# Kernel tuning notes

Hardware: AMD Instinct MI355X
Metric: run time of the kernel (lower is better)

## Reference

```python
import jax, jax.numpy as jnp
import numpy as np

# hyperparameters from init_kwargs
S = 1.0        # scale (fixed in module)
L = 0.5        # margin
W_EQ = 1.0
W_INEQ = 1.0

B, C, H, W, N_ANNOS = 32, 2, 480, 640, 4096


def setup_inputs() -> dict:
    key = jax.random.key(0)
    ks = jax.random.split(key, 8)
    prediction = jax.random.normal(ks[0], (B, C, H, W), dtype=jnp.float32)
    # targets columns: [class_a, x_a, y_a, class_b, x_b, y_b, label]
    ca = jax.random.randint(ks[1], (B, N_ANNOS), 0, C)
    xa = jax.random.randint(ks[2], (B, N_ANNOS), 0, W)
    ya = jax.random.randint(ks[3], (B, N_ANNOS), 0, H)
    cb = jax.random.randint(ks[4], (B, N_ANNOS), 0, C)
    xb = jax.random.randint(ks[5], (B, N_ANNOS), 0, W)
    yb = jax.random.randint(ks[6], (B, N_ANNOS), 0, H)
    lab = jax.random.randint(ks[7], (B, N_ANNOS), -1, 2)  # in {-1,0,1}
    targets = jnp.stack([ca, xa, ya, cb, xb, yb, lab], axis=-1).astype(jnp.int64)
    return {"prediction": prediction, "targets": targets}


def reference(prediction, targets):
    # prediction: [B, 2, H, W]; targets: [B, N, 7] int
    b_idx = jnp.arange(prediction.shape[0])[:, None]  # [B,1] broadcast over N
    # gather point-pair predictions: pred[b, class, row(y), col(x)]
    pa = prediction[b_idx, targets[:, :, 0], targets[:, :, 2], targets[:, :, 1]]  # [B,N]
    pb = prediction[b_idx, targets[:, :, 3], targets[:, :, 5], targets[:, :, 4]]  # [B,N]
    diff = pb - pa
    lab_i = targets[:, :, 6]
    lab = lab_i.astype(prediction.dtype)
    ineq_mask = lab_i != 0
    # squared hinge on inequality pairs, squared error on equality pairs
    loss_ineq = jnp.sum(jnp.square(jax.nn.relu(S * L - S * diff * lab)) * ineq_mask)
    loss_eq = jnp.sum(jnp.square(S * diff) * (~ineq_mask))
    num_ineq = jnp.sum(ineq_mask)
    num_eq = jnp.sum(~ineq_mask)
    norm_ineq = jnp.where(num_ineq > 0, 1.0 / jnp.maximum(num_ineq, 1), 0.0)
    norm_eq = jnp.where(num_eq > 0, 1.0 / jnp.maximum(num_eq, 1), 0.0)
    return W_INEQ * norm_ineq * loss_ineq + W_EQ * norm_eq * loss_eq
```

## Files before the change

### kernel.cpp

```cpp
#include <hip/hip_runtime.h>

#define BB 32
#define CC 2
#define HH 480
#define WW 640
#define NA 4096

struct Accum {
    double loss_ineq;
    double loss_eq;
    unsigned long long num_ineq;
};

__global__ __launch_bounds__(256) void lrizz_main(
        const float* __restrict__ pred,
        const int* __restrict__ tgt,
        Accum* __restrict__ acc) {
    const int total = BB * NA;
    int t = blockIdx.x * blockDim.x + threadIdx.x;

    float li = 0.f, le = 0.f;
    int ni = 0;

    if (t < total) {
        int b = t >> 12;
        const int* tp = tgt + (size_t)t * 7;
        int ca = tp[0], xa = tp[1], ya = tp[2];
        int cb = tp[3], xb = tp[4], yb = tp[5];
        int lab = tp[6];

        size_t base = (size_t)b * (CC * HH * WW);
        float pa = pred[base + ((size_t)ca * HH + (size_t)ya) * WW + (size_t)xa];
        float pb = pred[base + ((size_t)cb * HH + (size_t)yb) * WW + (size_t)xb];
        float diff = pb - pa;

        if (lab != 0) {
            float v = 0.5f - diff * (float)lab;
            v = fmaxf(v, 0.f);
            li = v * v;
            ni = 1;
        } else {
            le = diff * diff;
        }
    }

    #pragma unroll
    for (int off = 32; off > 0; off >>= 1) {
        li += __shfl_down(li, off, 64);
        le += __shfl_down(le, off, 64);
        ni += __shfl_down(ni, off, 64);
    }

    __shared__ float s_li[4], s_le[4];
    __shared__ int   s_ni[4];
    int wid  = threadIdx.x >> 6;
    int lane = threadIdx.x & 63;
    if (lane == 0) { s_li[wid] = li; s_le[wid] = le; s_ni[wid] = ni; }
    __syncthreads();

    if (threadIdx.x == 0) {
        float tli = s_li[0] + s_li[1] + s_li[2] + s_li[3];
        float tle = s_le[0] + s_le[1] + s_le[2] + s_le[3];
        int   tni = s_ni[0] + s_ni[1] + s_ni[2] + s_ni[3];
        atomicAdd(&acc->loss_ineq, (double)tli);
        atomicAdd(&acc->loss_eq,  (double)tle);
        atomicAdd(&acc->num_ineq, (unsigned long long)tni);
    }
}

__global__ void lrizz_final(const Accum* __restrict__ acc, float* __restrict__ out) {
    const double total = (double)(BB * NA);
    double ni = (double)acc->num_ineq;
    double ne = total - ni;
    double r = 0.0;
    if (ni > 0.0) r += acc->loss_ineq / ni;
    if (ne > 0.0) r += acc->loss_eq  / ne;
    out[0] = (float)r;
}

extern "C" void kernel_launch(void* const* d_in, const int* in_sizes, int n_in,
                              void* d_out, int out_size, void* d_ws, size_t ws_size,
                              hipStream_t stream) {
    const float* pred = (const float*)d_in[0];
    const int*   tgt  = (const int*)d_in[1];
    float* out = (float*)d_out;
    Accum* acc = (Accum*)d_ws;

    hipMemsetAsync(acc, 0, sizeof(Accum), stream);

    const int total = BB * NA;
    const int block = 256;
    const int grid  = total / block;
    lrizz_main<<<grid, block, 0, stream>>>(pred, tgt, acc);
    lrizz_final<<<1, 1, 0, stream>>>(acc, out);
}
```

Before: 124.3 us.

## Replace global atomics and memset with grid-stride partials and two-stage reduction

The main kernel now uses a fixed grid of 256 blocks with a grid-stride loop. Each block writes a float4 partial sum to workspace instead of issuing three double/u64 atomics per block. A 256-thread final kernel reduces the partials, and the memset launch is removed. The cost this targets is atomic contention and the extra memset launch. In exchange there is less memory-level parallelism per thread, and the count is now accumulated in float, which is exact at this size.

```diff
diff --git a/kernel.cpp b/kernel.cpp
--- a/kernel.cpp
+++ b/kernel.cpp
@@ -6,23 +6,19 @@
 #define WW 640
 #define NA 4096
 
-struct Accum {
-    double loss_ineq;
-    double loss_eq;
-    unsigned long long num_ineq;
-};
+#define GRID1 256
+#define BLOCK1 256
 
-__global__ __launch_bounds__(256) void lrizz_main(
+__global__ __launch_bounds__(BLOCK1) void lrizz_main(
         const float* __restrict__ pred,
         const int* __restrict__ tgt,
-        Accum* __restrict__ acc) {
+        float4* __restrict__ partials) {
     const int total = BB * NA;
-    int t = blockIdx.x * blockDim.x + threadIdx.x;
+    const int stride = GRID1 * BLOCK1;
 
-    float li = 0.f, le = 0.f;
-    int ni = 0;
+    float li = 0.f, le = 0.f, ni = 0.f;
 
-    if (t < total) {
+    for (int t = blockIdx.x * BLOCK1 + threadIdx.x; t < total; t += stride) {
         int b = t >> 12;
         const int* tp = tgt + (size_t)t * 7;
         int ca = tp[0], xa = tp[1], ya = tp[2];
@@ -35,12 +31,11 @@
         float diff = pb - pa;
 
         if (lab != 0) {
-            float v = 0.5f - diff * (float)lab;
-            v = fmaxf(v, 0.f);
-            li = v * v;
-            ni = 1;
+            float v = fmaxf(0.5f - diff * (float)lab, 0.f);
+            li += v * v;
+            ni += 1.f;
         } else {
-            le = diff * diff;
+            le += diff * diff;
         }
     }
 
@@ -51,31 +46,51 @@
         ni += __shfl_down(ni, off, 64);
     }
 
-    __shared__ float s_li[4], s_le[4];
-    __shared__ int   s_ni[4];
+    __shared__ float s_li[4], s_le[4], s_ni[4];
     int wid  = threadIdx.x >> 6;
     int lane = threadIdx.x & 63;
     if (lane == 0) { s_li[wid] = li; s_le[wid] = le; s_ni[wid] = ni; }
     __syncthreads();
 
     if (threadIdx.x == 0) {
-        float tli = s_li[0] + s_li[1] + s_li[2] + s_li[3];
-        float tle = s_le[0] + s_le[1] + s_le[2] + s_le[3];
-        int   tni = s_ni[0] + s_ni[1] + s_ni[2] + s_ni[3];
-        atomicAdd(&acc->loss_ineq, (double)tli);
-        atomicAdd(&acc->loss_eq,  (double)tle);
-        atomicAdd(&acc->num_ineq, (unsigned long long)tni);
+        float4 p;
+        p.x = s_li[0] + s_li[1] + s_li[2] + s_li[3];
+        p.y = s_le[0] + s_le[1] + s_le[2] + s_le[3];
+        p.z = s_ni[0] + s_ni[1] + s_ni[2] + s_ni[3];
+        p.w = 0.f;
+        partials[blockIdx.x] = p;
     }
 }
 
-__global__ void lrizz_final(const Accum* __restrict__ acc, float* __restrict__ out) {
-    const double total = (double)(BB * NA);
-    double ni = (double)acc->num_ineq;
-    double ne = total - ni;
-    double r = 0.0;
-    if (ni > 0.0) r += acc->loss_ineq / ni;
-    if (ne > 0.0) r += acc->loss_eq  / ne;
-    out[0] = (float)r;
+__global__ __launch_bounds__(GRID1) void lrizz_final(
+        const float4* __restrict__ partials,
+        float* __restrict__ out) {
+    float4 p = partials[threadIdx.x];
+    float li = p.x, le = p.y, ni = p.z;
+
+    #pragma unroll
+    for (int off = 32; off > 0; off >>= 1) {
+        li += __shfl_down(li, off, 64);
+        le += __shfl_down(le, off, 64);
+        ni += __shfl_down(ni, off, 64);
+    }
+
+    __shared__ float s_li[4], s_le[4], s_ni[4];
+    int wid  = threadIdx.x >> 6;
+    int lane = threadIdx.x & 63;
+    if (lane == 0) { s_li[wid] = li; s_le[wid] = le; s_ni[wid] = ni; }
+    __syncthreads();
+
+    if (threadIdx.x == 0) {
+        double tli = (double)(s_li[0] + s_li[1] + s_li[2] + s_li[3]);
+        double tle = (double)(s_le[0] + s_le[1] + s_le[2] + s_le[3]);
+        double tni = (double)(s_ni[0] + s_ni[1] + s_ni[2] + s_ni[3]);
+        double tne = (double)(BB * NA) - tni;
+        double r = 0.0;
+        if (tni > 0.0) r += tli / tni;
+        if (tne > 0.0) r += tle / tne;
+        out[0] = (float)r;
+    }
 }
 
 extern "C" void kernel_launch(void* const* d_in, const int* in_sizes, int n_in,
@@ -84,13 +99,8 @@
     const float* pred = (const float*)d_in[0];
     const int*   tgt  = (const int*)d_in[1];
     float* out = (float*)d_out;
-    Accum* acc = (Accum*)d_ws;
+    float4* partials = (float4*)d_ws;
 
-    hipMemsetAsync(acc, 0, sizeof(Accum), stream);
-
-    const int total = BB * NA;
-    const int block = 256;
-    const int grid  = total / block;
-    lrizz_main<<<grid, block, 0, stream>>>(pred, tgt, acc);
-    lrizz_final<<<1, 1, 0, stream>>>(acc, out);
+    lrizz_main<<<GRID1, BLOCK1, 0, stream>>>(pred, tgt, partials);
+    lrizz_final<<<1, GRID1, 0, stream>>>(partials, out);
 }
```

Result: faster. 106.1 us (-14.7%).
